# Kernel tuning notes

Measured on AMD Instinct MI355X. Metric: run time of the kernel, lower is better.

## Reference

```python
import jax, jax.numpy as jnp
import numpy as np

NUM_CLASSES = 64  # K: fill_max for class ids c


def setup_inputs() -> dict:
    key = jax.random.key(0)
    k1, k2 = jax.random.split(key)
    z = jax.random.normal(k1, (16, 8192, 256), dtype=jnp.float32)
    c = jax.random.randint(k2, (16, 8192), 0, NUM_CLASSES, dtype=jnp.int64)
    return {"z": z, "c": c}


def reference(z, c):
    # z: [B, S, D], c: [B, S] int class ids in [0, K)
    D = z.shape[-1]
    zf = z.reshape(-1, D)          # [N, D]
    cf = c.reshape(-1)             # [N]
    N = zf.shape[0]

    # Fused segmented reductions instead of a python loop over unique ids.
    counts = jax.ops.segment_sum(jnp.ones((N,), zf.dtype), cf, num_segments=NUM_CLASSES)  # [K]
    sums = jax.ops.segment_sum(zf, cf, num_segments=NUM_CLASSES)                          # [K, D]
    safe_counts = jnp.maximum(counts, 1.0)
    centroids = sums / safe_counts[:, None]                                               # [K, D] per-class mean

    # within-class variance: mean squared distance of members to their centroid
    diff = zf - centroids[cf]                                                             # [N, D] gather
    sq = jnp.sum(diff * diff, axis=-1)                                                    # [N]
    var_withins = jax.ops.segment_sum(sq, cf, num_segments=NUM_CLASSES) / safe_counts     # [K]

    return centroids, var_withins
```

## Files before the change

kernel.cpp:

```cpp
#include <hip/hip_runtime.h>
#include <hip/hip_bf16.h>

#define K_CLS 64
#define DIM   256
#define TPB1  512
#define MAXROWS 2048

typedef __attribute__((ext_vector_type(8)))  short short8;
typedef __attribute__((ext_vector_type(16))) float f32x16;
typedef __attribute__((ext_vector_type(4)))  unsigned int uint4v;

__device__ inline float bf2f(unsigned short h) {
    return __uint_as_float(((unsigned)h) << 16);
}
__device__ inline unsigned short f2bf(float x) {
    unsigned u = __float_as_uint(x);
    u += 0x7FFFu + ((u >> 16) & 1u);
    return (unsigned short)(u >> 16);
}
__device__ inline unsigned int pkbf(float lo, float hi) {
    float2 p; p.x = lo; p.y = hi;
    __hip_bfloat162 h = __float22bfloat162_rn(p);
    unsigned int r;
    __builtin_memcpy(&r, &h, sizeof(r));
    return r;
}

__global__ __launch_bounds__(TPB1) void fstat_p1(
    const float* __restrict__ z, const int* __restrict__ c,
    unsigned short* __restrict__ psum, unsigned short* __restrict__ psq,
    float* __restrict__ pcnt, int rows_per_blk, int nblk)
{
    __shared__ __align__(16) int cs[MAXROWS];
    __shared__ float lcnt[K_CLS];
    const int t   = threadIdx.x;
    const int blk = blockIdx.x;
    const int rb0 = blk * rows_per_blk;

    if (t < K_CLS) lcnt[t] = 0.f;
    __syncthreads();
    for (int r = t; r < rows_per_blk; r += TPB1) {
        int cv = c[rb0 + r];
        cs[r] = cv;
        atomicAdd(&lcnt[cv], 1.0f);
    }
    __syncthreads();

    const int wave = t >> 6;
    const int lane = t & 63;
    const int db   = wave * 32;
    const int half = lane >> 5;
    const int ln   = lane & 31;
    const int ln32 = ln + 32;

    f32x16 aS0 = {}; f32x16 aS1 = {}; f32x16 aQ0 = {}; f32x16 aQ1 = {};

    const int nsteps = rows_per_blk >> 4;
    const size_t zo0 = (size_t)(rb0 + half * 8) * DIM + db + ln;

    float v[8];
    #pragma unroll
    for (int i = 0; i < 8; ++i) v[i] = z[zo0 + (size_t)i * DIM];

    for (int step = 0; step < nsteps; ++step) {
        float vn[8];
        if (step + 1 < nsteps) {
            const size_t zo = zo0 + (size_t)(step + 1) * 16 * DIM;
            #pragma unroll
            for (int i = 0; i < 8; ++i) vn[i] = z[zo + (size_t)i * DIM];
        }
        const int rb = step * 16 + half * 8;
        int4 c0 = *reinterpret_cast<const int4*>(&cs[rb]);
        int4 c1 = *reinterpret_cast<const int4*>(&cs[rb + 4]);
        int cl[8] = {c0.x, c0.y, c0.z, c0.w, c1.x, c1.y, c1.z, c1.w};

        uint4v ua0, ua1, ubz, ubq;
        #pragma unroll
        for (int i = 0; i < 4; ++i) {
            int l0 = cl[2 * i], l1 = cl[2 * i + 1];
            ua0[i] = (l0 == ln   ? 0x00003F80u : 0u) | (l1 == ln   ? 0x3F800000u : 0u);
            ua1[i] = (l0 == ln32 ? 0x00003F80u : 0u) | (l1 == ln32 ? 0x3F800000u : 0u);
            float v0 = v[2 * i], v1 = v[2 * i + 1];
            ubz[i] = pkbf(v0, v1);
            ubq[i] = pkbf(v0 * v0, v1 * v1);
        }
        short8 A0 = __builtin_bit_cast(short8, ua0);
        short8 A1 = __builtin_bit_cast(short8, ua1);
        short8 Bz = __builtin_bit_cast(short8, ubz);
        short8 Bq = __builtin_bit_cast(short8, ubq);

        aS0 = __builtin_amdgcn_mfma_f32_32x32x16_bf16(A0, Bz, aS0, 0, 0, 0);
        aS1 = __builtin_amdgcn_mfma_f32_32x32x16_bf16(A1, Bz, aS1, 0, 0, 0);
        aQ0 = __builtin_amdgcn_mfma_f32_32x32x16_bf16(A0, Bq, aQ0, 0, 0, 0);
        aQ1 = __builtin_amdgcn_mfma_f32_32x32x16_bf16(A1, Bq, aQ1, 0, 0, 0);
        if (step + 1 < nsteps) {
            #pragma unroll
            for (int i = 0; i < 8; ++i) v[i] = vn[i];
        }
    }

    unsigned short* ps = psum + (size_t)blk * K_CLS * DIM;
    unsigned short* pq = psq  + (size_t)blk * K_CLS * DIM;
    #pragma unroll
    for (int r = 0; r < 16; ++r) {
        int row = (r & 3) + 8 * (r >> 2) + 4 * half;
        size_t o0 = (size_t)row * DIM + db + ln;
        size_t o1 = (size_t)(row + 32) * DIM + db + ln;
        ps[o0] = f2bf(aS0[r]); ps[o1] = f2bf(aS1[r]);
        pq[o0] = f2bf(aQ0[r]); pq[o1] = f2bf(aQ1[r]);
    }
    __syncthreads();
    if (t < K_CLS) pcnt[(size_t)t * nblk + blk] = lcnt[t];
}

__global__ __launch_bounds__(1024) void fstat_p2(
    const unsigned short* __restrict__ psum, const unsigned short* __restrict__ psq,
    const float* __restrict__ pcnt, float* __restrict__ out,
    float* __restrict__ wvar, float* __restrict__ wcnt, int nblk)
{
    const int k  = blockIdx.x >> 2;
    const int q  = blockIdx.x & 3;
    const int t  = threadIdx.x;
    const int d  = t & 63;
    const int sg = t >> 6;

    __shared__ float redS[16][64];
    __shared__ float redQ[16][64];
    __shared__ float redC[256];
    __shared__ float sh_cnt;

    if (t < 256) redC[t] = (t < nblk) ? pcnt[(size_t)k * nblk + t] : 0.f;
    __syncthreads();
    if (t < 64) {
        float cp = redC[t] + redC[t + 64] + redC[t + 128] + redC[t + 192];
        #pragma unroll
        for (int off = 32; off > 0; off >>= 1) cp += __shfl_down(cp, off);
        if (t == 0) sh_cnt = cp;
    }

    float s = 0.f, qq = 0.f;
    for (int b = sg; b < nblk; b += 16) {
        size_t o = ((size_t)b * K_CLS + k) * DIM + q * 64 + d;
        s  += bf2f(psum[o]);
        qq += bf2f(psq[o]);
    }
    redS[sg][d] = s;
    redQ[sg][d] = qq;
    __syncthreads();

    if (t < 64) {
        float su = 0.f, qu = 0.f;
        #pragma unroll
        for (int i = 0; i < 16; ++i) { su += redS[i][t]; qu += redQ[i][t]; }
        float cnt = fmaxf(sh_cnt, 1.f);
        float mu  = su / cnt;
        out[(size_t)k * DIM + q * 64 + t] = mu;
        float vp = qu - cnt * mu * mu;
        #pragma unroll
        for (int off = 32; off > 0; off >>= 1) vp += __shfl_down(vp, off);
        if (t == 0) {
            wvar[k * 4 + q] = vp;
            if (q == 0) wcnt[k] = sh_cnt;
        }
    }
}

__global__ void fstat_p3(const float* __restrict__ wvar,
                         const float* __restrict__ wcnt, float* __restrict__ out)
{
    int k = threadIdx.x;
    if (k < K_CLS) {
        float cnt = fmaxf(wcnt[k], 1.f);
        out[K_CLS * DIM + k] =
            (wvar[4 * k] + wvar[4 * k + 1] + wvar[4 * k + 2] + wvar[4 * k + 3]) / cnt;
    }
}

extern "C" void kernel_launch(void* const* d_in, const int* in_sizes, int n_in,
                              void* d_out, int out_size, void* d_ws, size_t ws_size,
                              hipStream_t stream)
{
    const float* z = (const float*)d_in[0];
    const int*   c = (const int*)d_in[1];
    float* out = (float*)d_out;
    const int N = in_sizes[1];

    auto need = [](int nb) {
        return 2 * (size_t)nb * K_CLS * DIM * sizeof(unsigned short)
             + (size_t)K_CLS * nb * sizeof(float)
             + (size_t)(K_CLS * 4 + K_CLS) * sizeof(float);
    };
    int nblk = 256;
    while (nblk > 64 &&
           (N % nblk != 0 || (N / nblk) % 16 != 0 || (N / nblk) > MAXROWS ||
            need(nblk) > ws_size))
        nblk >>= 1;

    const int rows_per_blk = N / nblk;

    unsigned short* psum = (unsigned short*)d_ws;
    unsigned short* psq  = psum + (size_t)nblk * K_CLS * DIM;
    float* pcnt = (float*)(psq + (size_t)nblk * K_CLS * DIM);
    float* wvar = pcnt + (size_t)K_CLS * nblk;
    float* wcnt = wvar + K_CLS * 4;

    fstat_p1<<<nblk, TPB1, 0, stream>>>(z, c, psum, psq, pcnt, rows_per_blk, nblk);
    fstat_p2<<<K_CLS * 4, 1024, 0, stream>>>(psum, psq, pcnt, out, wvar, wcnt, nblk);
    fstat_p3<<<1, K_CLS, 0, stream>>>(wvar, wcnt, out);
}
```

Measured before the change: 36.58 us.

## Split rows across two wave groups per block and merge partials in LDS

```diff
diff --git a/kernel.cpp b/kernel.cpp
--- a/kernel.cpp
+++ b/kernel.cpp
@@ -3,7 +3,7 @@
 
 #define K_CLS 64
 #define DIM   256
-#define TPB1  512
+#define TPB1  1024
 #define MAXROWS 2048
 
 typedef __attribute__((ext_vector_type(8)))  short short8;
@@ -33,6 +33,7 @@
 {
     __shared__ __align__(16) int cs[MAXROWS];
     __shared__ float lcnt[K_CLS];
+    __shared__ float lmg[K_CLS * DIM];
     const int t   = threadIdx.x;
     const int blk = blockIdx.x;
     const int rb0 = blk * rows_per_blk;
@@ -46,17 +47,21 @@
     }
     __syncthreads();
 
-    const int wave = t >> 6;
-    const int lane = t & 63;
-    const int db   = wave * 32;
-    const int half = lane >> 5;
-    const int ln   = lane & 31;
-    const int ln32 = ln + 32;
+    const int wave  = t >> 6;
+    const int lane  = t & 63;
+    const int slice = wave & 7;
+    const int h2    = wave >> 3;
+    const int db    = slice * 32;
+    const int half  = lane >> 5;
+    const int ln    = lane & 31;
+    const int ln32  = ln + 32;
 
     f32x16 aS0 = {}; f32x16 aS1 = {}; f32x16 aQ0 = {}; f32x16 aQ1 = {};
 
-    const int nsteps = rows_per_blk >> 4;
-    const size_t zo0 = (size_t)(rb0 + half * 8) * DIM + db + ln;
+    const int halfrows = rows_per_blk >> 1;
+    const int rbase    = h2 * halfrows;
+    const int nsteps   = halfrows >> 4;
+    const size_t zo0   = (size_t)(rb0 + rbase + half * 8) * DIM + db + ln;
 
     float v[8];
     #pragma unroll
@@ -69,7 +74,7 @@
             #pragma unroll
             for (int i = 0; i < 8; ++i) vn[i] = z[zo + (size_t)i * DIM];
         }
-        const int rb = step * 16 + half * 8;
+        const int rb = rbase + step * 16 + half * 8;
         int4 c0 = *reinterpret_cast<const int4*>(&cs[rb]);
         int4 c1 = *reinterpret_cast<const int4*>(&cs[rb + 4]);
         int cl[8] = {c0.x, c0.y, c0.z, c0.w, c1.x, c1.y, c1.z, c1.w};
@@ -101,15 +106,46 @@
 
     unsigned short* ps = psum + (size_t)blk * K_CLS * DIM;
     unsigned short* pq = psq  + (size_t)blk * K_CLS * DIM;
-    #pragma unroll
-    for (int r = 0; r < 16; ++r) {
-        int row = (r & 3) + 8 * (r >> 2) + 4 * half;
-        size_t o0 = (size_t)row * DIM + db + ln;
-        size_t o1 = (size_t)(row + 32) * DIM + db + ln;
-        ps[o0] = f2bf(aS0[r]); ps[o1] = f2bf(aS1[r]);
-        pq[o0] = f2bf(aQ0[r]); pq[o1] = f2bf(aQ1[r]);
-    }
-    __syncthreads();
+
+    if (h2 == 1) {
+        #pragma unroll
+        for (int r = 0; r < 16; ++r) {
+            int row = (r & 3) + 8 * (r >> 2) + 4 * half;
+            lmg[(size_t)row * DIM + db + ln]        = aS0[r];
+            lmg[(size_t)(row + 32) * DIM + db + ln] = aS1[r];
+        }
+    }
+    __syncthreads();
+    if (h2 == 0) {
+        #pragma unroll
+        for (int r = 0; r < 16; ++r) {
+            int row = (r & 3) + 8 * (r >> 2) + 4 * half;
+            size_t o0 = (size_t)row * DIM + db + ln;
+            size_t o1 = (size_t)(row + 32) * DIM + db + ln;
+            ps[o0] = f2bf(aS0[r] + lmg[o0]);
+            ps[o1] = f2bf(aS1[r] + lmg[o1]);
+        }
+    }
+    __syncthreads();
+    if (h2 == 1) {
+        #pragma unroll
+        for (int r = 0; r < 16; ++r) {
+            int row = (r & 3) + 8 * (r >> 2) + 4 * half;
+            lmg[(size_t)row * DIM + db + ln]        = aQ0[r];
+            lmg[(size_t)(row + 32) * DIM + db + ln] = aQ1[r];
+        }
+    }
+    __syncthreads();
+    if (h2 == 0) {
+        #pragma unroll
+        for (int r = 0; r < 16; ++r) {
+            int row = (r & 3) + 8 * (r >> 2) + 4 * half;
+            size_t o0 = (size_t)row * DIM + db + ln;
+            size_t o1 = (size_t)(row + 32) * DIM + db + ln;
+            pq[o0] = f2bf(aQ0[r] + lmg[o0]);
+            pq[o1] = f2bf(aQ1[r] + lmg[o1]);
+        }
+    }
     if (t < K_CLS) pcnt[(size_t)t * nblk + blk] = lcnt[t];
 }
 
@@ -192,7 +228,7 @@
     };
     int nblk = 256;
     while (nblk > 64 &&
-           (N % nblk != 0 || (N / nblk) % 16 != 0 || (N / nblk) > MAXROWS ||
+           (N % nblk != 0 || (N / nblk) % 32 != 0 || (N / nblk) > MAXROWS ||
             need(nblk) > ws_size))
         nblk >>= 1;
 
```

Measured after the change: 39.59 us. 8.2% more time.
